# Kernel tuning notes

Measured on AMD Instinct MI355X. Metric: run time of the kernel, lower is better.

The kernel has to match this reference:

```python
import jax, jax.numpy as jnp
import numpy as np

PATCHES = [(4, 4), (2, 2)]  # (width, height) per stream chunk
SCALE = 2
DM = 256


def conv2d(x, w, bias, pad=0):
    y = jax.lax.conv_general_dilated(
        x, w, window_strides=(1, 1), padding=[(pad, pad), (pad, pad)],
        dimension_numbers=("NCHW", "OIHW", "NCHW"))
    return y + bias[None, :, None, None]


def to_patches(x, b, t, dk, out_h, ph, out_w, pw):
    # x: [b*t, dk, out_h*ph, out_w*pw] -> [b, t*out_h*out_w, dk*ph*pw]
    x = x.reshape(b, t, dk, out_h, ph, out_w, pw)
    return x.transpose(0, 1, 3, 5, 2, 4, 6).reshape(b, t * out_h * out_w, dk * ph * pw)


def from_patches(y, b, t, dk, out_h, ph, out_w, pw):
    # y: [b, t*out_h*out_w, dk*ph*pw] -> [b*t, dk, out_h*ph, out_w*pw]
    y = y.reshape(b, t, out_h, out_w, dk, ph, pw)
    return y.transpose(0, 1, 4, 2, 5, 3, 6).reshape(b * t, dk, out_h * ph, out_w * pw)


def attention(q, k, v):
    d = q.shape[-1]
    scores = jnp.einsum("bnd,bmd->bnm", q, k) / jnp.sqrt(jnp.asarray(d, q.dtype))
    p = jax.nn.softmax(scores, axis=-1)
    return jnp.einsum("bnm,bmd->bnd", p, v)


def forward(x_lo, x_hi, b,
            wq_lo, bq_lo, wk_lo, bk_lo, wv_lo, bv_lo,
            wq_hi, bq_hi, wk_hi, bk_hi, wv_hi, bv_hi,
            wo_lo, bo_lo, wo_hi, bo_hi):
    bt_lo, _, h, w = x_lo.shape
    bt_hi, _, h_, w_ = x_hi.shape
    t_lo = bt_lo // b
    t_hi = bt_hi // b
    n_p = len(PATCHES)
    d_k_lo = DM * SCALE ** 2 // n_p
    d_k_hi = DM // n_p

    q_lo_all = conv2d(x_lo, wq_lo, bq_lo)
    k_lo_all = conv2d(x_lo, wk_lo, bk_lo)
    v_lo_all = conv2d(x_lo, wv_lo, bv_lo)
    q_hi_all = conv2d(x_hi, wq_hi, bq_hi)
    k_hi_all = conv2d(x_hi, wk_hi, bk_hi)
    v_hi_all = conv2d(x_hi, wv_hi, bv_hi)

    outs_lo, outs_hi = [], []
    for i, (width, height) in enumerate(PATCHES):
        out_w, out_h = w // width, h // height
        sl_lo = slice(i * d_k_lo, (i + 1) * d_k_lo)
        sl_hi = slice(i * d_k_hi, (i + 1) * d_k_hi)
        ql = to_patches(q_lo_all[:, sl_lo], b, t_lo, d_k_lo, out_h, height, out_w, width)
        kl = to_patches(k_lo_all[:, sl_lo], b, t_lo, d_k_lo, out_h, height, out_w, width)
        vl = to_patches(v_lo_all[:, sl_lo], b, t_lo, d_k_lo, out_h, height, out_w, width)
        qh = to_patches(q_hi_all[:, sl_hi], b, t_hi, d_k_hi, out_h, height * SCALE, out_w, width * SCALE)
        kh = to_patches(k_hi_all[:, sl_hi], b, t_hi, d_k_hi, out_h, height * SCALE, out_w, width * SCALE)
        vh = to_patches(v_hi_all[:, sl_hi], b, t_hi, d_k_hi, out_h, height * SCALE, out_w, width * SCALE)

        q = jnp.concatenate([ql, qh], axis=1)
        k = jnp.concatenate([kl, kh], axis=1)
        v = jnp.concatenate([vl, vh], axis=1)
        y = attention(q, k, v)

        n_lo = t_lo * out_h * out_w
        y_lo = from_patches(y[:, :n_lo], b, t_lo, d_k_lo, out_h, height, out_w, width)
        y_hi = from_patches(y[:, n_lo:], b, t_hi, d_k_hi, out_h, height * SCALE, out_w, width * SCALE)
        outs_lo.append(y_lo)
        outs_hi.append(y_hi)

    out_lo = jnp.concatenate(outs_lo, axis=1)
    out_hi = jnp.concatenate(outs_hi, axis=1)
    out_lo = jax.nn.leaky_relu(conv2d(out_lo, wo_lo, bo_lo, pad=1), 0.2)
    out_hi = jax.nn.leaky_relu(conv2d(out_hi, wo_hi, bo_hi, pad=1), 0.2)
    return out_lo, out_hi


def setup_inputs() -> dict:
    key = jax.random.key(0)
    ks = jax.random.split(key, 12)
    dm2 = DM * SCALE ** 2  # 1024
    s = 0.02
    inp = {
        "x_lo": jax.random.normal(ks[0], (16, DM, 32, 32), jnp.float32),
        "x_hi": jax.random.normal(ks[1], (16, DM, 64, 64), jnp.float32),
        "b": 4,
        "wq_lo": jax.random.normal(ks[2], (dm2, DM, 1, 1), jnp.float32) * s,
        "bq_lo": jnp.zeros((dm2,), jnp.float32),
        "wk_lo": jax.random.normal(ks[3], (dm2, DM, 1, 1), jnp.float32) * s,
        "bk_lo": jnp.zeros((dm2,), jnp.float32),
        "wv_lo": jax.random.normal(ks[4], (dm2, DM, 1, 1), jnp.float32) * s,
        "bv_lo": jnp.zeros((dm2,), jnp.float32),
        "wq_hi": jax.random.normal(ks[5], (DM, DM, 1, 1), jnp.float32) * s,
        "bq_hi": jnp.zeros((DM,), jnp.float32),
        "wk_hi": jax.random.normal(ks[6], (DM, DM, 1, 1), jnp.float32) * s,
        "bk_hi": jnp.zeros((DM,), jnp.float32),
        "wv_hi": jax.random.normal(ks[7], (DM, DM, 1, 1), jnp.float32) * s,
        "bv_hi": jnp.zeros((DM,), jnp.float32),
        "wo_lo": jax.random.normal(ks[8], (DM, dm2, 3, 3), jnp.float32) * s,
        "bo_lo": jnp.zeros((DM,), jnp.float32),
        "wo_hi": jax.random.normal(ks[9], (DM, DM, 3, 3), jnp.float32) * s,
        "bo_hi": jnp.zeros((DM,), jnp.float32),
    }
    return inp


def reference(x_lo, x_hi, b,
              wq_lo, bq_lo, wk_lo, bk_lo, wv_lo, bv_lo,
              wq_hi, bq_hi, wk_hi, bk_hi, wv_hi, bv_hi,
              wo_lo, bo_lo, wo_hi, bo_hi):
    return forward(x_lo, x_hi, b,
                   wq_lo, bq_lo, wk_lo, bk_lo, wv_lo, bv_lo,
                   wq_hi, bq_hi, wk_hi, bk_hi, wv_hi, bv_hi,
                   wo_lo, bo_lo, wo_hi, bo_hi)
```

## Files before the change

### kernel.cpp

```cpp
#include <hip/hip_runtime.h>
#include <hip/hip_bf16.h>
#include <stdint.h>

typedef __attribute__((ext_vector_type(8))) short short8;
typedef __attribute__((ext_vector_type(4))) short short4v;
typedef __attribute__((ext_vector_type(2))) short short2v;
typedef __attribute__((ext_vector_type(4))) float floatx4;

__device__ __forceinline__ unsigned short f2b(float f) {
  unsigned u = __builtin_bit_cast(unsigned, f);
  unsigned r = u + 0x7fffu + ((u >> 16) & 1u);
  return (unsigned short)(r >> 16);
}
__device__ __forceinline__ float b2f(unsigned short h) {
  unsigned u = ((unsigned)h) << 16;
  return __builtin_bit_cast(float, u);
}
__device__ __forceinline__ void glds16(const unsigned short* src, unsigned short* dst) {
  __builtin_amdgcn_global_load_lds((const __attribute__((address_space(1))) void*)src,
                                   (__attribute__((address_space(3))) void*)dst, 16, 0, 0);
}
__device__ __forceinline__ int swz(int r, int o) {
  return (r << 9) + (o ^ ((((o >> 7) & 3) ^ (r & 7)) << 4));
}
__device__ __forceinline__ void xcd_remap(int& bx, int& by, int& bz) {
  const int gx = gridDim.x, gy = gridDim.y;
  const int nwg = gx * gy * (int)gridDim.z;
  int lin = bx + gx * (by + gy * bz);
  lin = (lin & 7) * (nwg >> 3) + (lin >> 3);
  bx = lin % gx; const int r = lin / gx;
  by = r % gy; bz = r / gy;
}

struct GemmP {
  const unsigned short* A;
  const unsigned short* B;
  long sAb, sBb;
  int lda, ldb, K;
  unsigned short* C; long sCb; int ldc;
  const float* bias;
  unsigned short *Q0, *K0, *V0t, *Q1, *K1, *V1t;
};

template<int EPI>
__global__ __launch_bounds__(512) void gemm256(GemmP p) {
  __shared__ __align__(16) unsigned short LDS[65536];
  const int tid = threadIdx.x;
  const int wv = tid >> 6, lane = tid & 63;
  const int wm = wv >> 2, wn = wv & 3;
  const int g = lane >> 4, l16 = lane & 15;
  int bx = blockIdx.x, by = blockIdx.y, bz = blockIdx.z;
  xcd_remap(bx, by, bz);
  const int m0 = by * 256, n0 = bx * 256;

  int bb = bz, koff = 0, Keff = p.K;
  if constexpr (EPI == 1) { bb = bz >> 4; koff = (bz & 15) * (p.K >> 4); Keff = p.K >> 4; }
  const unsigned short* Ab = p.A + (long)bb * p.sAb + (long)m0 * p.lda + koff;
  const unsigned short* Bb = p.B + (long)bb * p.sBb + (long)n0 * p.ldb + koff;
  const int NT = Keff >> 5;

  const int r0 = tid >> 2;
  const int cs = (tid & 3) ^ ((r0 >> 1) & 3);
  const unsigned short* aS0 = Ab + (long)r0 * p.lda + cs * 8;
  const unsigned short* aS1 = aS0 + (long)128 * p.lda;
  const unsigned short* bS0 = Bb + (long)r0 * p.ldb + cs * 8;
  const unsigned short* bS1 = bS0 + (long)128 * p.ldb;
  unsigned short* const lds0 = (unsigned short*)LDS;
  const int wbase = wv * 512;

  auto STAGE_A = [&](int t) {
    unsigned short* d = lds0 + (t & 3) * 16384;
    const long ko = (long)t * 32;
    glds16(aS0 + ko, d + wbase);
    glds16(aS1 + ko, d + 4096 + wbase);
  };
  auto STAGE_B = [&](int t) {
    unsigned short* d = lds0 + (t & 3) * 16384 + 8192;
    const long ko = (long)t * 32;
    glds16(bS0 + ko, d + wbase);
    glds16(bS1 + ko, d + 4096 + wbase);
  };

  STAGE_A(0); STAGE_B(0); STAGE_A(1); STAGE_B(1); STAGE_A(2); STAGE_B(2);

  floatx4 acc[8][4];
  const floatx4 z4 = {0.f, 0.f, 0.f, 0.f};
#pragma unroll
  for (int i = 0; i < 8; ++i)
#pragma unroll
    for (int j = 0; j < 4; ++j) acc[i][j] = z4;

  const int loff = l16 * 32 + ((g ^ ((l16 >> 1) & 3)) * 8);
  const int aRowB = wm * 128;

  asm volatile("s_waitcnt vmcnt(8)" ::: "memory");
  __builtin_amdgcn_s_barrier();
  short8 bf[4], af[4];
#pragma unroll
  for (int ni = 0; ni < 4; ++ni)
    bf[ni] = *(const short8*)(lds0 + 8192 + (wn * 64 + ni * 16) * 32 + loff);
#pragma unroll
  for (int mi = 0; mi < 4; ++mi)
    af[mi] = *(const short8*)(lds0 + (aRowB + mi * 16) * 32 + loff);

  for (int t = 0; t < NT; ++t) {
    const unsigned short* As = lds0 + (t & 3) * 16384;
    const unsigned short* AsN = lds0 + ((t + 1) & 3) * 16384;
    if (t < NT - 2) asm volatile("s_waitcnt vmcnt(4)" ::: "memory");
    else            asm volatile("s_waitcnt vmcnt(0)" ::: "memory");
    __builtin_amdgcn_s_barrier();
    __builtin_amdgcn_sched_barrier(0);
    if (t + 3 < NT) STAGE_A(t + 3);
    short8 ag[4];
#pragma unroll
    for (int mi = 0; mi < 4; ++mi)
      ag[mi] = *(const short8*)(As + (aRowB + 64 + mi * 16) * 32 + loff);
    __builtin_amdgcn_s_setprio(1);
#pragma unroll
    for (int mi = 0; mi < 4; ++mi)
#pragma unroll
      for (int ni = 0; ni < 4; ++ni)
        acc[mi][ni] = __builtin_amdgcn_mfma_f32_16x16x32_bf16(af[mi], bf[ni], acc[mi][ni], 0, 0, 0);
    __builtin_amdgcn_s_setprio(0);
    if (t + 3 < NT) STAGE_B(t + 3);
    short8 bfN[4], afN[4];
    if (t + 1 < NT) {
      const unsigned short* BsN = AsN + 8192;
#pragma unroll
      for (int ni = 0; ni < 4; ++ni)
        bfN[ni] = *(const short8*)(BsN + (wn * 64 + ni * 16) * 32 + loff);
#pragma unroll
      for (int mi = 0; mi < 4; ++mi)
        afN[mi] = *(const short8*)(AsN + (aRowB + mi * 16) * 32 + loff);
    }
    __builtin_amdgcn_s_setprio(1);
#pragma unroll
    for (int mi = 0; mi < 4; ++mi)
#pragma unroll
      for (int ni = 0; ni < 4; ++ni)
        acc[4 + mi][ni] = __builtin_amdgcn_mfma_f32_16x16x32_bf16(ag[mi], bf[ni], acc[4 + mi][ni], 0, 0, 0);
    __builtin_amdgcn_s_setprio(0);
    if (t + 1 < NT) {
#pragma unroll
      for (int i = 0; i < 4; ++i) { bf[i] = bfN[i]; af[i] = afN[i]; }
    }
  }

  if constexpr (EPI == 1) {
    unsigned short* C = p.C + (long)bz * p.sCb;
#pragma unroll
    for (int mi = 0; mi < 8; ++mi) {
#pragma unroll
      for (int ni = 0; ni < 4; ++ni) {
        const int col = n0 + wn * 64 + ni * 16 + l16;
#pragma unroll
        for (int r4 = 0; r4 < 4; ++r4) {
          const int row = m0 + wm * 128 + mi * 16 + g * 4 + r4;
          C[(long)row * p.ldc + col] = f2b(acc[mi][ni][r4]);
        }
      }
    }
  } else {
    __syncthreads();
    char* shb = (char*)LDS;
    const int sel = (EPI == 2) ? (m0 >> 10) : (m0 >> 8);
#pragma unroll
    for (int mi = 0; mi < 8; ++mi) {
#pragma unroll
      for (int ni = 0; ni < 4; ++ni) {
        const int c = wn * 64 + ni * 16 + l16;
#pragma unroll
        for (int r4 = 0; r4 < 4; ++r4) {
          const int rr = wm * 128 + mi * 16 + g * 4 + r4;
          float v = acc[mi][ni][r4];
          if constexpr (EPI == 2 || EPI == 3) {
            v += p.bias[m0 + rr];
            if (sel == 0) {
              float sc;
              if constexpr (EPI == 2) sc = ((m0 & 1023) < 512) ? 0.011048543456039806f
                                                               : 0.02209708691207961f;
              else                    sc = (rr < 128) ? 0.011048543456039806f
                                                      : 0.02209708691207961f;
              v *= sc;
            }
          }
          *(unsigned short*)(shb + swz(rr, c * 2)) = f2b(v);
        }
      }
    }
    __syncthreads();

    if constexpr (EPI == 0) {
      unsigned short* C = p.C + (long)bz * p.sCb;
#pragma unroll
      for (int j = 0; j < 16; ++j) {
        const int e = j * 512 + tid;
        const int r = e >> 5, ck = e & 31;
        short8 v = *(const short8*)(shb + swz(r, ck * 16));
        *(short8*)(C + (long)(m0 + r) * p.ldc + n0 + ck * 8) = v;
      }
    } else if constexpr (EPI == 2) {
      const int chb = m0 & 1023;
      const bool cfg0 = chb < 512;
      const int b = bz >> 2, tt = bz & 3;
      const int k0 = n0 >> 8;
      unsigned short* dst = cfg0 ? (sel == 0 ? p.Q0 : sel == 1 ? p.K0 : p.V0t)
                                 : (sel == 0 ? p.Q1 : sel == 1 ? p.K1 : p.V1t);
      if (sel != 2) {
        if (cfg0) {
          const long base = (long)(b * 512) * 8192;
#pragma unroll
          for (int j = 0; j < 16; ++j) {
            const int e = j * 512 + tid;
            const int pi = e >> 9, idx2 = e & 511;
            const int ch = idx2 >> 1, hf = idx2 & 1;
            const int oyL = pi >> 3, ox = pi & 7;
            const int nseq = (tt * 8 + 2 * k0 + oyL) * 8 + ox;
            const int yl = oyL * 4 + hf * 2;
            short4v a = *(const short4v*)(shb + swz(ch, (yl * 32 + ox * 4) * 2));
            short4v b2 = *(const short4v*)(shb + swz(ch, ((yl + 1) * 32 + ox * 4) * 2));
            short8 v = {a[0], a[1], a[2], a[3], b2[0], b2[1], b2[2], b2[3]};
            *(short8*)(dst + base + (long)nseq * 8192 + (chb + ch) * 16 + hf * 8) = v;
          }
        } else {
          const int c2lo = chb - 512;
          const long base = (long)(b * 2048) * 2048;
#pragma unroll
          for (int j = 0; j < 16; ++j) {
            const int e = j * 512 + tid;
            const int pi = e >> 7, cp = e & 127;
            const int oyL = pi >> 4, ox = pi & 15;
            const int nseq = (tt * 16 + 4 * k0 + oyL) * 16 + ox;
            short8 v;
#pragma unroll
            for (int rr = 0; rr < 2; ++rr) {
#pragma unroll
              for (int k = 0; k < 2; ++k) {
                short2v pr = *(const short2v*)(shb +
                    swz(cp * 2 + rr, ((oyL * 2 + k) * 32 + ox * 2) * 2));
                v[rr * 4 + k * 2] = pr[0];
                v[rr * 4 + k * 2 + 1] = pr[1];
              }
            }
            *(short8*)(dst + base + (long)nseq * 2048 + (c2lo + cp * 2) * 4) = v;
          }
        }
      } else {
        if (cfg0) {
          const long base = (long)(b * 8192) * 512;
#pragma unroll
          for (int j = 0; j < 16; ++j) {
            const int e = j * 512 + tid;
            const int oyL = e >> 12, fu = e & 4095;
            const int ch = fu >> 4, pp = fu & 15;
            const int py = pp >> 2, px = pp & 3;
            const int yl = oyL * 4 + py;
            short8 v;
#pragma unroll
            for (int ox = 0; ox < 8; ++ox)
              v[ox] = *(const unsigned short*)(shb + swz(ch, (yl * 32 + ox * 4 + px) * 2));
            const long f = (long)(chb + ch) * 16 + pp;
            *(short8*)(dst + base + f * 512 + (tt * 8 + 2 * k0 + oyL) * 8) = v;
          }
        } else {
          const int c2lo = chb - 512;
          const long base = (long)(b * 2048) * 2048;
#pragma unroll
          for (int j = 0; j < 16; ++j) {
            const int e = j * 512 + tid;
            const int he = e & 1, oyL = (e >> 1) & 3, fu = e >> 3;
            const int c2 = fu >> 2, pp = fu & 3;
            const int py = pp >> 1, px = pp & 1;
            const int yl = oyL * 2 + py;
            short8 v;
#pragma unroll
            for (int i = 0; i < 8; ++i) {
              const int ox = he * 8 + i;
              v[i] = *(const unsigned short*)(shb + swz(c2, (yl * 32 + ox * 2 + px) * 2));
            }
            const long f = (long)(c2lo + c2) * 4 + pp;
            *(short8*)(dst + base + f * 2048 + (tt * 16 + 4 * k0 + oyL) * 16 + he * 8) = v;
          }
        }
      }
    } else if constexpr (EPI == 3) {
      const int b = bz >> 2, tt = bz & 3;
      const int k0 = n0 >> 8;
      const int oyA = k0 >> 1, pyb = (k0 & 1) * 4;
      unsigned short* dstA = sel == 0 ? p.Q0 : sel == 1 ? p.K0 : p.V0t;
      unsigned short* dstB = sel == 0 ? p.Q1 : sel == 1 ? p.K1 : p.V1t;
      if (sel != 2) {
#pragma unroll
        for (int j = 0; j < 16; ++j) {
          const int e = j * 512 + tid;
          if (e < 4096) {
            const int ox = e >> 9, cy = e & 511;
            const int ch = cy >> 2, yl = cy & 3;
            const int nseq = 256 + (tt * 8 + oyA) * 8 + ox;
            short8 v = *(const short8*)(shb + swz(ch, (yl * 64 + ox * 8) * 2));
            *(short8*)(dstA + ((long)(b * 512 + nseq)) * 8192 + ch * 64 + (pyb + yl) * 8) = v;
          } else {
            const int ee = e - 4096;
            const int ox = ee >> 8, cc = ee & 255;
            const int c2 = cc >> 1, hf = cc & 1;
            const int nseq = 1024 + (tt * 16 + k0) * 16 + ox;
            short8 v;
#pragma unroll
            for (int k = 0; k < 2; ++k) {
              short4v a = *(const short4v*)(shb +
                  swz(128 + c2, ((hf * 2 + k) * 64 + ox * 4) * 2));
              v[k * 4] = a[0]; v[k * 4 + 1] = a[1]; v[k * 4 + 2] = a[2]; v[k * 4 + 3] = a[3];
            }
            *(short8*)(dstB + ((long)(b * 2048 + nseq)) * 2048 + c2 * 16 + hf * 8) = v;
          }
        }
      } else {
#pragma unroll
        for (int j = 0; j < 16; ++j) {
          const int e = j * 512 + tid;
          if (e < 4096) {
            const int ch = e >> 5, yl = (e >> 3) & 3, px = e & 7;
            short8 v;
#pragma unroll
            for (int ox = 0; ox < 8; ++ox)
              v[ox] = *(const unsigned short*)(shb + swz(ch, (yl * 64 + ox * 8 + px) * 2));
            const long f = (long)ch * 64 + (pyb + yl) * 8 + px;
            *(short8*)(dstA + ((long)b * 8192 + f) * 512 + 256 + (tt * 8 + oyA) * 8) = v;
          } else {
            const int ee = e - 4096;
            const int he = ee & 1, fu = ee >> 1;
            const int c2 = fu >> 4, pp = fu & 15;
            const int py = pp >> 2, px = pp & 3;
            short8 v;
#pragma unroll
            for (int i = 0; i < 8; ++i) {
              const int x = (he * 8 + i) * 4 + px;
              v[i] = *(const unsigned short*)(shb + swz(128 + c2, (py * 64 + x) * 2));
            }
            const long f = (long)c2 * 16 + pp;
            *(short8*)(dstB + ((long)b * 2048 + f) * 2048 + 1024 + (tt * 16 + k0) * 16 + he * 8) = v;
          }
        }
      }
    }
  }
}

template<int H, int W, int CIN, int KS, bool PARTIAL>
__global__ __launch_bounds__(512) void conv256(const unsigned short* __restrict__ Cinp,
                                               const unsigned short* __restrict__ Wt,
                                               const float* __restrict__ bias,
                                               float* __restrict__ out,
                                               unsigned short* __restrict__ P0,
                                               unsigned short* __restrict__ P1) {
  constexpr int HP = H + 2, WP = W + 2;
  constexpr int CC = CIN / KS;
  constexpr int NT = 9 * CC / 32;
  __shared__ __align__(16) unsigned short LDS[65536];
  const int tid = threadIdx.x;
  const int wv = tid >> 6, lane = tid & 63;
  const int wm = wv >> 2, wn = wv & 3;
  const int g = lane >> 4, l16 = lane & 15;
  int bx = blockIdx.x, by = blockIdx.y, bz = blockIdx.z;
  xcd_remap(bx, by, bz);
  const int bt = bz / KS, ks = bz % KS;
  const int n0 = bx * 256;

  const int r0 = tid >> 2;
  const int cs = (tid & 3) ^ ((r0 >> 1) & 3);
  const unsigned short* wA0 = Wt + (long)r0 * CIN + ks * CC + cs * 8;
  const unsigned short* wA1 = wA0 + (long)128 * CIN;
  const int p0 = n0 + r0, p1 = p0 + 128;
  const int y0p = p0 / W, x0p = p0 % W;
  const int y1p = p1 / W, x1p = p1 % W;
  const unsigned short* cB = Cinp + (long)bt * HP * WP * CIN + ks * CC + cs * 8;
  const unsigned short* pB0 = cB + ((long)y0p * WP + x0p) * CIN;
  const unsigned short* pB1 = cB + ((long)y1p * WP + x1p) * CIN;
  unsigned short* const lds0 = (unsigned short*)LDS;
  const int wbase = wv * 512;

  auto STAGE_A = [&](int t) {
    unsigned short* d = lds0 + (t & 3) * 16384;
    const int tap = t >> 3, tc = (t & 7) * 32;
    const long off = (long)tap * (256L * CIN) + tc;
    glds16(wA0 + off, d + wbase);
    glds16(wA1 + off, d + 4096 + wbase);
  };
  auto STAGE_B = [&](int t) {
    unsigned short* d = lds0 + (t & 3) * 16384 + 8192;
    const int tap = t >> 3, tc = (t & 7) * 32;
    const int ky = tap / 3, kx = tap - ky * 3;
    const long off = ((long)ky * WP + kx) * CIN + tc;
    glds16(pB0 + off, d + wbase);
    glds16(pB1 + off, d + 4096 + wbase);
  };

  STAGE_A(0); STAGE_B(0); STAGE_A(1); STAGE_B(1); STAGE_A(2); STAGE_B(2);

  floatx4 acc[8][4];
  const floatx4 z4 = {0.f, 0.f, 0.f, 0.f};
#pragma unroll
  for (int i = 0; i < 8; ++i)
#pragma unroll
    for (int j = 0; j < 4; ++j) acc[i][j] = z4;

  const int loff = l16 * 32 + ((g ^ ((l16 >> 1) & 3)) * 8);
  const int aRowB = wm * 128;

  asm volatile("s_waitcnt vmcnt(8)" ::: "memory");
  __builtin_amdgcn_s_barrier();
  short8 bf[4], af[4];
#pragma unroll
  for (int ni = 0; ni < 4; ++ni)
    bf[ni] = *(const short8*)(lds0 + 8192 + (wn * 64 + ni * 16) * 32 + loff);
#pragma unroll
  for (int mi = 0; mi < 4; ++mi)
    af[mi] = *(const short8*)(lds0 + (aRowB + mi * 16) * 32 + loff);

  for (int t = 0; t < NT; ++t) {
    const unsigned short* As = lds0 + (t & 3) * 16384;
    const unsigned short* AsN = lds0 + ((t + 1) & 3) * 16384;
    if (t < NT - 2) asm volatile("s_waitcnt vmcnt(4)" ::: "memory");
    else            asm volatile("s_waitcnt vmcnt(0)" ::: "memory");
    __builtin_amdgcn_s_barrier();
    __builtin_amdgcn_sched_barrier(0);
    if (t + 3 < NT) STAGE_A(t + 3);
    short8 ag[4];
#pragma unroll
    for (int mi = 0; mi < 4; ++mi)
      ag[mi] = *(const short8*)(As + (aRowB + 64 + mi * 16) * 32 + loff);
    __builtin_amdgcn_s_setprio(1);
#pragma unroll
    for (int mi = 0; mi < 4; ++mi)
#pragma unroll
      for (int ni = 0; ni < 4; ++ni)
        acc[mi][ni] = __builtin_amdgcn_mfma_f32_16x16x32_bf16(af[mi], bf[ni], acc[mi][ni], 0, 0, 0);
    __builtin_amdgcn_s_setprio(0);
    if (t + 3 < NT) STAGE_B(t + 3);
    short8 bfN[4], afN[4];
    if (t + 1 < NT) {
      const unsigned short* BsN = AsN + 8192;
#pragma unroll
      for (int ni = 0; ni < 4; ++ni)
        bfN[ni] = *(const short8*)(BsN + (wn * 64 + ni * 16) * 32 + loff);
#pragma unroll
      for (int mi = 0; mi < 4; ++mi)
        afN[mi] = *(const short8*)(AsN + (aRowB + mi * 16) * 32 + loff);
    }
    __builtin_amdgcn_s_setprio(1);
#pragma unroll
    for (int mi = 0; mi < 4; ++mi)
#pragma unroll
      for (int ni = 0; ni < 4; ++ni)
        acc[4 + mi][ni] = __builtin_amdgcn_mfma_f32_16x16x32_bf16(ag[mi], bf[ni], acc[4 + mi][ni], 0, 0, 0);
    __builtin_amdgcn_s_setprio(0);
    if (t + 1 < NT) {
#pragma unroll
      for (int i = 0; i < 4; ++i) { bf[i] = bfN[i]; af[i] = afN[i]; }
    }
  }

  if constexpr (!PARTIAL) {
#pragma unroll
    for (int mi = 0; mi < 8; ++mi) {
#pragma unroll
      for (int ni = 0; ni < 4; ++ni) {
        const int pn = n0 + wn * 64 + ni * 16 + l16;
        const int y = pn / W, x = pn % W;
#pragma unroll
        for (int r4 = 0; r4 < 4; ++r4) {
          const int co = wm * 128 + mi * 16 + g * 4 + r4;
          float v = acc[mi][ni][r4] + bias[co];
          v = v > 0.f ? v : 0.2f * v;
          out[(((long)bt * 256 + co) * H + y) * W + x] = v;
        }
      }
    }
  } else {
    unsigned short* pout = (ks < 2 ? P0 : P1) + (long)(ks & 1) * (16L * 256 * H * W);
#pragma unroll
    for (int mi = 0; mi < 8; ++mi) {
#pragma unroll
      for (int ni = 0; ni < 4; ++ni) {
        const int pn = n0 + wn * 64 + ni * 16 + l16;
        const int y = pn / W, x = pn % W;
#pragma unroll
        for (int r4 = 0; r4 < 4; ++r4) {
          const int co = wm * 128 + mi * 16 + g * 4 + r4;
          pout[(((long)bt * 256 + co) * H + y) * W + x] = f2b(acc[mi][ni][r4]);
        }
      }
    }
  }
}

template<int L>
__global__ __launch_bounds__(256) void softmax_rows(unsigned short* S) {
  const int w = threadIdx.x >> 6, lane = threadIdx.x & 63;
  const long row = (long)blockIdx.x * 4 + w;
  unsigned short* R = S + row * L;
  constexpr int NC = L / 64;
  float v[NC];
  float m = -1e30f;
#pragma unroll
  for (int i = 0; i < NC; ++i) { v[i] = b2f(R[i * 64 + lane]); m = fmaxf(m, v[i]); }
#pragma unroll
  for (int off = 32; off; off >>= 1) m = fmaxf(m, __shfl_xor(m, off, 64));
  float s = 0.f;
#pragma unroll
  for (int i = 0; i < NC; ++i) { v[i] = __expf(v[i] - m); s += v[i]; }
#pragma unroll
  for (int off = 32; off; off >>= 1) s += __shfl_xor(s, off, 64);
  const float inv = 1.0f / s;
#pragma unroll
  for (int i = 0; i < NC; ++i) R[i * 64 + lane] = f2b(v[i] * inv);
}

__global__ __launch_bounds__(256) void softmax_red16(const unsigned short* __restrict__ P,
                                                     unsigned short* __restrict__ S) {
  const int w = threadIdx.x >> 6, lane = threadIdx.x & 63;
  const int rowg = blockIdx.x * 4 + w;
  const int b = rowg >> 9, n = rowg & 511;
  const unsigned short* base = P + ((long)b * 16) * 262144 + (long)n * 512 + lane;
  float v[8];
#pragma unroll
  for (int i = 0; i < 8; ++i) {
    float s = 0.f;
#pragma unroll
    for (int ks = 0; ks < 16; ++ks) s += b2f(base[(long)ks * 262144 + i * 64]);
    v[i] = s;
  }
  float m = -1e30f;
#pragma unroll
  for (int i = 0; i < 8; ++i) m = fmaxf(m, v[i]);
#pragma unroll
  for (int off = 32; off; off >>= 1) m = fmaxf(m, __shfl_xor(m, off, 64));
  float s = 0.f;
#pragma unroll
  for (int i = 0; i < 8; ++i) { v[i] = __expf(v[i] - m); s += v[i]; }
#pragma unroll
  for (int off = 32; off; off >>= 1) s += __shfl_xor(s, off, 64);
  const float inv = 1.0f / s;
  unsigned short* R = S + (long)rowg * 512;
#pragma unroll
  for (int i = 0; i < 8; ++i) R[i * 64 + lane] = f2b(v[i] * inv);
}

__global__ __launch_bounds__(256) void xt_kernel(const float* __restrict__ x,
                                                 unsigned short* __restrict__ xt, int NPIX) {
  __shared__ unsigned short tile[64 * 65];
  const int tid = threadIdx.x;
  const int bt = blockIdx.z, ch0 = blockIdx.y * 64;
  const long pix0 = (long)blockIdx.x * 64;
  const float* src = x + ((long)bt * 256 + ch0) * NPIX + pix0;
#pragma unroll
  for (int i = 0; i < 16; ++i) {
    const int lin = i * 256 + tid;
    const int ch = lin >> 6, px = lin & 63;
    tile[ch * 65 + px] = f2b(src[(long)ch * NPIX + px]);
  }
  __syncthreads();
  unsigned short* dst = xt + ((long)bt * NPIX + pix0) * 256 + ch0;
#pragma unroll
  for (int i = 0; i < 16; ++i) {
    const int lin = i * 256 + tid;
    const int px = lin >> 6, ch = lin & 63;
    dst[(long)px * 256 + ch] = tile[ch * 65 + px];
  }
}

__global__ void prep_qkv_w(const float* wq, const float* wk, const float* wv,
                           const float* bq, const float* bk, const float* bv,
                           unsigned short* Wcat, float* Bcat, int CO) {
  const int idx = blockIdx.x * 256 + threadIdx.x;
  const int n = 3 * CO * 256;
  if (idx < n) {
    const int sel = idx / (CO * 256);
    const int r = idx - sel * CO * 256;
    const float* wsel = sel == 0 ? wq : (sel == 1 ? wk : wv);
    Wcat[idx] = f2b(wsel[r]);
  }
  if (idx < 3 * CO) {
    const int sel = idx / CO;
    const int r = idx - sel * CO;
    const float* bsel = sel == 0 ? bq : (sel == 1 ? bk : bv);
    Bcat[idx] = bsel[r];
  }
}

template<int CIN, int OC>
__global__ __launch_bounds__(256) void prep_conv_w2(const float* __restrict__ wo,
                                                    unsigned short* __restrict__ Wt) {
  __shared__ unsigned short T[9 * OC * CIN];
  const int o0 = blockIdx.x * OC;
  const int tid = threadIdx.x;
  constexpr int N = OC * CIN * 9;
  const float* src = wo + (long)o0 * CIN * 9;
  for (int j = tid; j < N; j += 256) {
    const int t9 = j % 9;
    const int r = j / 9;
    T[t9 * (OC * CIN) + r] = f2b(src[j]);
  }
  __syncthreads();
#pragma unroll
  for (int t9 = 0; t9 < 9; ++t9) {
    for (int j = tid; j < OC * CIN; j += 256) {
      const int oo = j / CIN, i = j - oo * CIN;
      Wt[((long)t9 * 256 + o0 + oo) * CIN + i] = T[t9 * (OC * CIN) + j];
    }
  }
}

__global__ __launch_bounds__(256) void zero_border(unsigned short* buf, int HP, int WP, int C) {
  const long i = (long)blockIdx.x * 256 + threadIdx.x;
  const int per_px = C >> 3;
  const int strip = 2 * WP + 2 * (HP - 2);
  const long tot = (long)16 * strip * per_px;
  if (i >= tot) return;
  const int c8 = (int)(i % per_px);
  const long r = i / per_px;
  const int s = (int)(r % strip);
  const int bt = (int)(r / strip);
  int y, x;
  if (s < WP) { y = 0; x = s; }
  else if (s < 2 * WP) { y = HP - 1; x = s - WP; }
  else if (s < 2 * WP + (HP - 2)) { y = s - 2 * WP + 1; x = 0; }
  else { y = s - 2 * WP - (HP - 2) + 1; x = WP - 1; }
  const short8 z = {0, 0, 0, 0, 0, 0, 0, 0};
  *(short8*)(buf + (((long)bt * HP + y) * WP + x) * C + c8 * 8) = z;
}

__global__ __launch_bounds__(256) void repackY0(const unsigned short* __restrict__ Y0,
                                                unsigned short* __restrict__ CinLo,
                                                unsigned short* __restrict__ CinHi) {
  __shared__ __align__(16) unsigned short T[8704];
  const int r = blockIdx.x;
  const int b = r >> 9, n = r & 511;
  const int tid = threadIdx.x;
  const int wv2 = tid >> 6, lane = tid & 63;
  const unsigned short* row = Y0 + (long)r * 8192;
  if (n < 256) {
#pragma unroll
    for (int q = 0; q < 4; ++q) {
      short8 v = *(const short8*)(row + tid * 32 + q * 8);
#pragma unroll
      for (int j = 0; j < 8; ++j) {
        const int f = tid * 32 + q * 8 + j;
        T[(f & 15) * 520 + (f >> 4)] = (unsigned short)v[j];
      }
    }
    __syncthreads();
    const int t = n >> 6, oh = (n >> 3) & 7, ow = n & 7;
    const int bt = b * 4 + t;
#pragma unroll
    for (int it = 0; it < 4; ++it) {
      const int pp = it * 4 + wv2;
      const int py = pp >> 2, px = pp & 3;
      short8 v = *(const short8*)(T + pp * 520 + lane * 8);
      *(short8*)(CinLo + (((long)bt * 34 + oh * 4 + py + 1) * 34 + ow * 4 + px + 1) * 1024
                 + lane * 8) = v;
    }
  } else {
    const int m = n - 256;
#pragma unroll
    for (int q = 0; q < 4; ++q) {
      short8 v = *(const short8*)(row + tid * 32 + q * 8);
#pragma unroll
      for (int j = 0; j < 8; ++j) {
        const int f = tid * 32 + q * 8 + j;
        T[(f & 63) * 136 + (f >> 6)] = (unsigned short)v[j];
      }
    }
    __syncthreads();
    const int t = m >> 6, oh = (m >> 3) & 7, ow = m & 7;
    const int bt = b * 4 + t;
#pragma unroll
    for (int it = 0; it < 4; ++it) {
      const int pp = it * 16 + wv2 * 4 + (lane >> 4);
      const int py = pp >> 3, px = pp & 7;
      short8 v = *(const short8*)(T + pp * 136 + (lane & 15) * 8);
      *(short8*)(CinHi + (((long)bt * 66 + oh * 8 + py + 1) * 66 + ow * 8 + px + 1) * 256
                 + (lane & 15) * 8) = v;
    }
  }
}

__global__ __launch_bounds__(256) void repackY1(const unsigned short* __restrict__ Y1,
                                                unsigned short* __restrict__ CinLo,
                                                unsigned short* __restrict__ CinHi) {
  __shared__ __align__(16) unsigned short T[2176];
  const int r = blockIdx.x;
  const int b = r >> 11, n = r & 2047;
  const int tid = threadIdx.x;
  const int wv2 = tid >> 6, lane = tid & 63;
  const unsigned short* row = Y1 + (long)r * 2048;
  short8 v = *(const short8*)(row + tid * 8);
  if (n < 1024) {
#pragma unroll
    for (int j = 0; j < 8; ++j) {
      const int f = tid * 8 + j;
      T[(f & 3) * 520 + (f >> 2)] = (unsigned short)v[j];
    }
    __syncthreads();
    const int t = n >> 8, oh = (n >> 4) & 15, ow = n & 15;
    const int bt = b * 4 + t;
    const int pp = wv2, py = pp >> 1, px = pp & 1;
    short8 o = *(const short8*)(T + pp * 520 + lane * 8);
    *(short8*)(CinLo + (((long)bt * 34 + oh * 2 + py + 1) * 34 + ow * 2 + px + 1) * 1024
               + 512 + lane * 8) = o;
  } else {
    const int m = n - 1024;
#pragma unroll
    for (int j = 0; j < 8; ++j) {
      const int f = tid * 8 + j;
      T[(f & 15) * 136 + (f >> 4)] = (unsigned short)v[j];
    }
    __syncthreads();
    const int t = m >> 8, oh = (m >> 4) & 15, ow = m & 15;
    const int bt = b * 4 + t;
    const int pp = wv2 * 4 + (lane >> 4), py = pp >> 2, px = pp & 3;
    short8 o = *(const short8*)(T + pp * 136 + (lane & 15) * 8);
    *(short8*)(CinHi + (((long)bt * 66 + oh * 4 + py + 1) * 66 + ow * 4 + px + 1) * 256
               + 128 + (lane & 15) * 8) = o;
  }
}

__global__ __launch_bounds__(256) void reduce_lrelu(const unsigned short* __restrict__ P0,
                                                    const unsigned short* __restrict__ P1,
                                                    const float* __restrict__ bias,
                                                    float* __restrict__ out) {
  const long i = (long)blockIdx.x * 256 + threadIdx.x;
  const long flat = i * 8;
  constexpr long SL = 4194304;
  short8 a = *(const short8*)(P0 + flat);
  short8 b = *(const short8*)(P0 + SL + flat);
  short8 c = *(const short8*)(P1 + flat);
  short8 d = *(const short8*)(P1 + SL + flat);
  const int co = ((int)(flat >> 10)) & 255;
  const float bv = bias[co];
  floatx4 r0, r1;
#pragma unroll
  for (int j = 0; j < 8; ++j) {
    float v = b2f((unsigned short)a[j]) + b2f((unsigned short)b[j]) +
              b2f((unsigned short)c[j]) + b2f((unsigned short)d[j]) + bv;
    v = v > 0.f ? v : 0.2f * v;
    if (j < 4) r0[j] = v; else r1[j - 4] = v;
  }
  *(floatx4*)(out + flat) = r0;
  *(floatx4*)(out + flat + 4) = r1;
}

extern "C" void kernel_launch(void* const* d_in, const int* in_sizes, int n_in,
                              void* d_out, int out_size, void* d_ws, size_t ws_size,
                              hipStream_t stream) {
  (void)in_sizes; (void)n_in; (void)out_size; (void)ws_size;
  const float* x_lo = (const float*)d_in[0];
  const float* x_hi = (const float*)d_in[1];
  const float* wq_lo = (const float*)d_in[3];
  const float* bq_lo = (const float*)d_in[4];
  const float* wk_lo = (const float*)d_in[5];
  const float* bk_lo = (const float*)d_in[6];
  const float* wv_lo = (const float*)d_in[7];
  const float* bv_lo = (const float*)d_in[8];
  const float* wq_hi = (const float*)d_in[9];
  const float* bq_hi = (const float*)d_in[10];
  const float* wk_hi = (const float*)d_in[11];
  const float* bk_hi = (const float*)d_in[12];
  const float* wv_hi = (const float*)d_in[13];
  const float* bv_hi = (const float*)d_in[14];
  const float* wo_lo = (const float*)d_in[15];
  const float* bo_lo = (const float*)d_in[16];
  const float* wo_hi = (const float*)d_in[17];
  const float* bo_hi = (const float*)d_in[18];
  float* out = (float*)d_out;

  char* ws = (char*)d_ws;
  const long B0 = 33554432;
  unsigned short* Qp0 = (unsigned short*)(ws);
  unsigned short* Kp0 = (unsigned short*)(ws + B0);
  unsigned short* V0t = (unsigned short*)(ws + 2 * B0);
  unsigned short* Qp1 = (unsigned short*)(ws + 3 * B0);
  unsigned short* Kp1 = (unsigned short*)(ws + 4 * B0);
  unsigned short* V1t = (unsigned short*)(ws + 5 * B0);
  char* ptr = ws + 6 * B0;
  unsigned short* S0 = (unsigned short*)ptr;     ptr += 2097152;
  unsigned short* Xt_lo = (unsigned short*)ptr;  ptr += 8388608;
  unsigned short* Xt_hi = (unsigned short*)ptr;  ptr += 33554432;
  unsigned short* Wcat_lo = (unsigned short*)ptr; ptr += 1572864;
  unsigned short* Wcat_hi = (unsigned short*)ptr; ptr += 393216;
  float* Bcat_lo = (float*)ptr;                  ptr += 12288;
  float* Bcat_hi = (float*)ptr;                  ptr += 3072;
  unsigned short* Wt_lo = (unsigned short*)ptr;  ptr += 4718592;
  unsigned short* Wt_hi = (unsigned short*)ptr;  ptr += 1179648;
  unsigned short* S1 = Kp0;
  unsigned short* Y0 = Qp0;
  unsigned short* Y1 = Qp1;
  unsigned short* CinP_lo = Kp0;
  unsigned short* CinP_hi = Kp1;
  unsigned short* S0p = Xt_hi;
  unsigned short* PC0 = Qp0;
  unsigned short* PC1 = Qp1;

  prep_qkv_w<<<(3 * 1024 * 256 + 255) / 256, 256, 0, stream>>>(
      wq_lo, wk_lo, wv_lo, bq_lo, bk_lo, bv_lo, Wcat_lo, Bcat_lo, 1024);
  prep_qkv_w<<<(3 * 256 * 256 + 255) / 256, 256, 0, stream>>>(
      wq_hi, wk_hi, wv_hi, bq_hi, bk_hi, bv_hi, Wcat_hi, Bcat_hi, 256);
  prep_conv_w2<1024, 1><<<256, 256, 0, stream>>>(wo_lo, Wt_lo);
  prep_conv_w2<256, 4><<<64, 256, 0, stream>>>(wo_hi, Wt_hi);
  xt_kernel<<<dim3(16, 4, 16), 256, 0, stream>>>(x_lo, Xt_lo, 1024);
  xt_kernel<<<dim3(64, 4, 16), 256, 0, stream>>>(x_hi, Xt_hi, 4096);

  {
    GemmP p{};
    p.A = Wcat_lo; p.B = Xt_lo; p.sAb = 0; p.sBb = 1024L * 256;
    p.lda = 256; p.ldb = 256; p.K = 256;
    p.bias = Bcat_lo;
    p.Q0 = Qp0; p.K0 = Kp0; p.V0t = V0t; p.Q1 = Qp1; p.K1 = Kp1; p.V1t = V1t;
    gemm256<2><<<dim3(4, 12, 16), 512, 0, stream>>>(p);
    p.A = Wcat_hi; p.B = Xt_hi; p.sBb = 4096L * 256; p.bias = Bcat_hi;
    gemm256<3><<<dim3(16, 3, 16), 512, 0, stream>>>(p);
  }

  {
    GemmP s{};
    s.A = Qp0; s.B = Kp0; s.sAb = 512L * 8192; s.sBb = 512L * 8192;
    s.lda = 8192; s.ldb = 8192; s.K = 8192;
    s.C = S0p; s.sCb = 262144; s.ldc = 512;
    gemm256<1><<<dim3(2, 2, 64), 512, 0, stream>>>(s);
    softmax_red16<<<512, 256, 0, stream>>>(S0p, S0);
    GemmP pv{};
    pv.A = S0; pv.B = V0t; pv.sAb = 512L * 512; pv.sBb = 8192L * 512;
    pv.lda = 512; pv.ldb = 512; pv.K = 512;
    pv.C = Y0; pv.sCb = 512L * 8192; pv.ldc = 8192;
    gemm256<0><<<dim3(32, 2, 4), 512, 0, stream>>>(pv);
  }

  {
    GemmP s{};
    s.A = Qp1; s.B = Kp1; s.sAb = 2048L * 2048; s.sBb = 2048L * 2048;
    s.lda = 2048; s.ldb = 2048; s.K = 2048;
    s.C = S1; s.sCb = 2048L * 2048; s.ldc = 2048;
    gemm256<0><<<dim3(8, 8, 4), 512, 0, stream>>>(s);
    softmax_rows<2048><<<2048, 256, 0, stream>>>(S1);
    GemmP pv{};
    pv.A = S1; pv.B = V1t; pv.sAb = 2048L * 2048; pv.sBb = 2048L * 2048;
    pv.lda = 2048; pv.ldb = 2048; pv.K = 2048;
    pv.C = Y1; pv.sCb = 2048L * 2048; pv.ldc = 2048;
    gemm256<0><<<dim3(8, 8, 4), 512, 0, stream>>>(pv);
  }

  zero_border<<<1056, 256, 0, stream>>>(CinP_lo, 34, 34, 1024);
  zero_border<<<520, 256, 0, stream>>>(CinP_hi, 66, 66, 256);
  repackY0<<<2048, 256, 0, stream>>>(Y0, CinP_lo, CinP_hi);
  repackY1<<<8192, 256, 0, stream>>>(Y1, CinP_lo, CinP_hi);

  conv256<32, 32, 1024, 4, true><<<dim3(4, 1, 64), 512, 0, stream>>>(
      CinP_lo, Wt_lo, bo_lo, out, PC0, PC1);
  reduce_lrelu<<<2048, 256, 0, stream>>>(PC0, PC1, bo_lo, out);
  conv256<64, 64, 256, 1, false><<<dim3(16, 1, 16), 512, 0, stream>>>(
      CinP_hi, Wt_hi, bo_hi, out + 4194304, nullptr, nullptr);
}
```

Before: 552.8 us.

## Fuse PV GEMM epilogues with padded-conv-input repack, drop repack kernels

Adds two GEMM epilogue modes that scatter the attention PV results straight into the zero-padded NHWC conv input buffers, replacing the separate repackY0/repackY1 kernels. Workspace aliasing is rearranged so the conv inputs live in the Q buffers and the partial-sum buffers in the V buffers. This removes a full write and read of the intermediate attention outputs and two kernel launches. In exchange the epilogue stores become scattered, with 8-byte stores in one path, which may make the GEMM tail slower.

```diff
diff --git a/kernel.cpp b/kernel.cpp
--- a/kernel.cpp
+++ b/kernel.cpp
@@ -340,6 +340,82 @@
             const long f = (long)c2 * 16 + pp;
             *(short8*)(dstB + ((long)b * 2048 + f) * 2048 + 1024 + (tt * 16 + k0) * 16 + he * 8) = v;
           }
+        }
+      }
+    } else if constexpr (EPI == 4) {
+      const int b = bz;
+      if (m0 == 0) {
+        const int chbase = n0 >> 4;
+        unsigned short* dst = p.Q0;
+#pragma unroll
+        for (int j = 0; j < 16; ++j) {
+          const int e = j * 512 + tid;
+          const int hf = e & 1, pp = (e >> 1) & 15, rr = e >> 5;
+          const int t = rr >> 6, oh = (rr >> 3) & 7, ow = rr & 7;
+          const int bt = b * 4 + t;
+          const int py = pp >> 2, px = pp & 3;
+          short8 v;
+#pragma unroll
+          for (int i = 0; i < 8; ++i)
+            v[i] = *(const unsigned short*)(shb + swz(rr, ((hf * 8 + i) * 16 + pp) * 2));
+          *(short8*)(dst + (((long)bt * 34 + oh * 4 + py + 1) * 34 + ow * 4 + px + 1) * 1024
+                     + chbase + hf * 8) = v;
+        }
+      } else {
+        const int chbase = n0 >> 6;
+        unsigned short* dst = p.Q1;
+#pragma unroll
+        for (int j = 0; j < 32; ++j) {
+          const int e = j * 512 + tid;
+          const int pp = e & 63, rr = e >> 6;
+          const int t = rr >> 6, oh = (rr >> 3) & 7, ow = rr & 7;
+          const int bt = b * 4 + t;
+          const int py = pp >> 3, px = pp & 7;
+          short4v v;
+#pragma unroll
+          for (int i = 0; i < 4; ++i)
+            v[i] = *(const unsigned short*)(shb + swz(rr, (i * 64 + pp) * 2));
+          *(short4v*)(dst + (((long)bt * 66 + oh * 8 + py + 1) * 66 + ow * 8 + px + 1) * 256
+                      + chbase) = v;
+        }
+      }
+    } else if constexpr (EPI == 5) {
+      const int b = bz;
+      if (m0 < 1024) {
+        const int chbase = n0 >> 2;
+        unsigned short* dst = p.Q0;
+#pragma unroll
+        for (int j = 0; j < 16; ++j) {
+          const int e = j * 512 + tid;
+          const int ch8 = e & 7, pp = (e >> 3) & 3, rr = e >> 5;
+          const int n = m0 + rr;
+          const int t = n >> 8, oh = (n >> 4) & 15, ow = n & 15;
+          const int bt = b * 4 + t;
+          const int py = pp >> 1, px = pp & 1;
+          short8 v;
+#pragma unroll
+          for (int i = 0; i < 8; ++i)
+            v[i] = *(const unsigned short*)(shb + swz(rr, ((ch8 * 8 + i) * 4 + pp) * 2));
+          *(short8*)(dst + (((long)bt * 34 + oh * 2 + py + 1) * 34 + ow * 2 + px + 1) * 1024
+                     + 512 + chbase + ch8 * 8) = v;
+        }
+      } else {
+        const int chbase = n0 >> 4;
+        unsigned short* dst = p.Q1;
+#pragma unroll
+        for (int j = 0; j < 16; ++j) {
+          const int e = j * 512 + tid;
+          const int hf = e & 1, pp = (e >> 1) & 15, rr = e >> 5;
+          const int m = m0 + rr - 1024;
+          const int t = m >> 8, oh = (m >> 4) & 15, ow = m & 15;
+          const int bt = b * 4 + t;
+          const int py = pp >> 2, px = pp & 3;
+          short8 v;
+#pragma unroll
+          for (int i = 0; i < 8; ++i)
+            v[i] = *(const unsigned short*)(shb + swz(rr, ((hf * 8 + i) * 16 + pp) * 2));
+          *(short8*)(dst + (((long)bt * 66 + oh * 4 + py + 1) * 66 + ow * 4 + px + 1) * 256
+                     + 128 + chbase + hf * 8) = v;
         }
       }
     }
@@ -628,101 +704,6 @@
   else { y = s - 2 * WP - (HP - 2) + 1; x = WP - 1; }
   const short8 z = {0, 0, 0, 0, 0, 0, 0, 0};
   *(short8*)(buf + (((long)bt * HP + y) * WP + x) * C + c8 * 8) = z;
-}
-
-__global__ __launch_bounds__(256) void repackY0(const unsigned short* __restrict__ Y0,
-                                                unsigned short* __restrict__ CinLo,
-                                                unsigned short* __restrict__ CinHi) {
-  __shared__ __align__(16) unsigned short T[8704];
-  const int r = blockIdx.x;
-  const int b = r >> 9, n = r & 511;
-  const int tid = threadIdx.x;
-  const int wv2 = tid >> 6, lane = tid & 63;
-  const unsigned short* row = Y0 + (long)r * 8192;
-  if (n < 256) {
-#pragma unroll
-    for (int q = 0; q < 4; ++q) {
-      short8 v = *(const short8*)(row + tid * 32 + q * 8);
-#pragma unroll
-      for (int j = 0; j < 8; ++j) {
-        const int f = tid * 32 + q * 8 + j;
-        T[(f & 15) * 520 + (f >> 4)] = (unsigned short)v[j];
-      }
-    }
-    __syncthreads();
-    const int t = n >> 6, oh = (n >> 3) & 7, ow = n & 7;
-    const int bt = b * 4 + t;
-#pragma unroll
-    for (int it = 0; it < 4; ++it) {
-      const int pp = it * 4 + wv2;
-      const int py = pp >> 2, px = pp & 3;
-      short8 v = *(const short8*)(T + pp * 520 + lane * 8);
-      *(short8*)(CinLo + (((long)bt * 34 + oh * 4 + py + 1) * 34 + ow * 4 + px + 1) * 1024
-                 + lane * 8) = v;
-    }
-  } else {
-    const int m = n - 256;
-#pragma unroll
-    for (int q = 0; q < 4; ++q) {
-      short8 v = *(const short8*)(row + tid * 32 + q * 8);
-#pragma unroll
-      for (int j = 0; j < 8; ++j) {
-        const int f = tid * 32 + q * 8 + j;
-        T[(f & 63) * 136 + (f >> 6)] = (unsigned short)v[j];
-      }
-    }
-    __syncthreads();
-    const int t = m >> 6, oh = (m >> 3) & 7, ow = m & 7;
-    const int bt = b * 4 + t;
-#pragma unroll
-    for (int it = 0; it < 4; ++it) {
-      const int pp = it * 16 + wv2 * 4 + (lane >> 4);
-      const int py = pp >> 3, px = pp & 7;
-      short8 v = *(const short8*)(T + pp * 136 + (lane & 15) * 8);
-      *(short8*)(CinHi + (((long)bt * 66 + oh * 8 + py + 1) * 66 + ow * 8 + px + 1) * 256
-                 + (lane & 15) * 8) = v;
-    }
-  }
-}
-
-__global__ __launch_bounds__(256) void repackY1(const unsigned short* __restrict__ Y1,
-                                                unsigned short* __restrict__ CinLo,
-                                                unsigned short* __restrict__ CinHi) {
-  __shared__ __align__(16) unsigned short T[2176];
-  const int r = blockIdx.x;
-  const int b = r >> 11, n = r & 2047;
-  const int tid = threadIdx.x;
-  const int wv2 = tid >> 6, lane = tid & 63;
-  const unsigned short* row = Y1 + (long)r * 2048;
-  short8 v = *(const short8*)(row + tid * 8);
-  if (n < 1024) {
-#pragma unroll
-    for (int j = 0; j < 8; ++j) {
-      const int f = tid * 8 + j;
-      T[(f & 3) * 520 + (f >> 2)] = (unsigned short)v[j];
-    }
-    __syncthreads();
-    const int t = n >> 8, oh = (n >> 4) & 15, ow = n & 15;
-    const int bt = b * 4 + t;
-    const int pp = wv2, py = pp >> 1, px = pp & 1;
-    short8 o = *(const short8*)(T + pp * 520 + lane * 8);
-    *(short8*)(CinLo + (((long)bt * 34 + oh * 2 + py + 1) * 34 + ow * 2 + px + 1) * 1024
-               + 512 + lane * 8) = o;
-  } else {
-    const int m = n - 1024;
-#pragma unroll
-    for (int j = 0; j < 8; ++j) {
-      const int f = tid * 8 + j;
-      T[(f & 15) * 136 + (f >> 4)] = (unsigned short)v[j];
-    }
-    __syncthreads();
-    const int t = m >> 8, oh = (m >> 4) & 15, ow = m & 15;
-    const int bt = b * 4 + t;
-    const int pp = wv2 * 4 + (lane >> 4), py = pp >> 2, px = pp & 3;
-    short8 o = *(const short8*)(T + pp * 136 + (lane & 15) * 8);
-    *(short8*)(CinHi + (((long)bt * 66 + oh * 4 + py + 1) * 66 + ow * 4 + px + 1) * 256
-               + 128 + (lane & 15) * 8) = o;
-  }
 }
 
 __global__ __launch_bounds__(256) void reduce_lrelu(const unsigned short* __restrict__ P0,
@@ -792,14 +773,12 @@
   float* Bcat_hi = (float*)ptr;                  ptr += 3072;
   unsigned short* Wt_lo = (unsigned short*)ptr;  ptr += 4718592;
   unsigned short* Wt_hi = (unsigned short*)ptr;  ptr += 1179648;
-  unsigned short* S1 = Kp0;
-  unsigned short* Y0 = Qp0;
-  unsigned short* Y1 = Qp1;
-  unsigned short* CinP_lo = Kp0;
-  unsigned short* CinP_hi = Kp1;
   unsigned short* S0p = Xt_hi;
-  unsigned short* PC0 = Qp0;
-  unsigned short* PC1 = Qp1;
+  unsigned short* S1 = Xt_hi;
+  unsigned short* CinP_lo = Qp0;
+  unsigned short* CinP_hi = Qp1;
+  unsigned short* PC0 = V0t;
+  unsigned short* PC1 = V1t;
 
   prep_qkv_w<<<(3 * 1024 * 256 + 255) / 256, 256, 0, stream>>>(
       wq_lo, wk_lo, wv_lo, bq_lo, bk_lo, bv_lo, Wcat_lo, Bcat_lo, 1024);
@@ -828,11 +807,6 @@
     s.C = S0p; s.sCb = 262144; s.ldc = 512;
     gemm256<1><<<dim3(2, 2, 64), 512, 0, stream>>>(s);
     softmax_red16<<<512, 256, 0, stream>>>(S0p, S0);
-    GemmP pv{};
-    pv.A = S0; pv.B = V0t; pv.sAb = 512L * 512; pv.sBb = 8192L * 512;
-    pv.lda = 512; pv.ldb = 512; pv.K = 512;
-    pv.C = Y0; pv.sCb = 512L * 8192; pv.ldc = 8192;
-    gemm256<0><<<dim3(32, 2, 4), 512, 0, stream>>>(pv);
   }
 
   {
@@ -842,17 +816,24 @@
     s.C = S1; s.sCb = 2048L * 2048; s.ldc = 2048;
     gemm256<0><<<dim3(8, 8, 4), 512, 0, stream>>>(s);
     softmax_rows<2048><<<2048, 256, 0, stream>>>(S1);
+  }
+
+  zero_border<<<1056, 256, 0, stream>>>(CinP_lo, 34, 34, 1024);
+  zero_border<<<520, 256, 0, stream>>>(CinP_hi, 66, 66, 256);
+  {
+    GemmP pv{};
+    pv.A = S0; pv.B = V0t; pv.sAb = 512L * 512; pv.sBb = 8192L * 512;
+    pv.lda = 512; pv.ldb = 512; pv.K = 512;
+    pv.Q0 = CinP_lo; pv.Q1 = CinP_hi;
+    gemm256<4><<<dim3(32, 2, 4), 512, 0, stream>>>(pv);
+  }
+  {
     GemmP pv{};
     pv.A = S1; pv.B = V1t; pv.sAb = 2048L * 2048; pv.sBb = 2048L * 2048;
     pv.lda = 2048; pv.ldb = 2048; pv.K = 2048;
-    pv.C = Y1; pv.sCb = 2048L * 2048; pv.ldc = 2048;
-    gemm256<0><<<dim3(8, 8, 4), 512, 0, stream>>>(pv);
-  }
-
-  zero_border<<<1056, 256, 0, stream>>>(CinP_lo, 34, 34, 1024);
-  zero_border<<<520, 256, 0, stream>>>(CinP_hi, 66, 66, 256);
-  repackY0<<<2048, 256, 0, stream>>>(Y0, CinP_lo, CinP_hi);
-  repackY1<<<8192, 256, 0, stream>>>(Y1, CinP_lo, CinP_hi);
+    pv.Q0 = CinP_lo; pv.Q1 = CinP_hi;
+    gemm256<5><<<dim3(8, 8, 4), 512, 0, stream>>>(pv);
+  }
 
   conv256<32, 32, 1024, 4, true><<<dim3(4, 1, 64), 512, 0, stream>>>(
       CinP_lo, Wt_lo, bo_lo, out, PC0, PC1);
```

Measured after the change: 551.0 us. Within noise of the previous version (-0.3%).
